# Performance work log

Hardware: AMD Instinct MI355X
Metric: run time of the kernel (lower is better)

The kernel has to match this reference:

```python
import jax, jax.numpy as jnp
import numpy as np

RX = 2  # matches init rx
RY = 2  # matches init ry


def _bilinear_gather(img, coords):
    """Bilinear sample with zero padding (mirrors grid_sample align_corners=True, padding_mode='zeros').
    img: [C,H,W]; coords: [P,2] pixel-space (x,y). Returns [C,P]."""
    C, H, W = img.shape
    x, y = coords[:, 0], coords[:, 1]
    x0, y0 = jnp.floor(x), jnp.floor(y)
    wx, wy = x - x0, y - y0

    def tap(xi, yi, w):
        valid = (xi >= 0) & (xi <= W - 1) & (yi >= 0) & (yi <= H - 1)
        xc = jnp.clip(xi, 0, W - 1).astype(jnp.int32)
        yc = jnp.clip(yi, 0, H - 1).astype(jnp.int32)
        v = img[:, yc, xc]  # [C,P] gather
        return v * (w * valid.astype(w.dtype))[None, :]

    return (tap(x0, y0, (1 - wx) * (1 - wy)) + tap(x0 + 1, y0, wx * (1 - wy))
            + tap(x0, y0 + 1, (1 - wx) * wy) + tap(x0 + 1, y0 + 1, wx * wy))


def _local_cost_volume(flow, f1, f2, rx, ry):
    """build_sample_cv: windowed bilinear gather of f2 around (grid + flow), dot with f1.
    Returns cv [N,H,W,2ry+1,2rx+1] with window ordered (dy,dx)."""
    N, C, H, W = f1.shape
    dt = f1.dtype
    gy, gx = jnp.meshgrid(jnp.arange(H, dtype=dt), jnp.arange(W, dtype=dt), indexing='ij')
    base = jnp.stack([gx, gy], 0)[None]            # [1,2,H,W] (x,y) like coords_grid
    cen = (base + flow).transpose(0, 2, 3, 1)       # [N,H,W,2]
    dx = jnp.linspace(-rx, rx, 2 * rx + 1).astype(dt)
    dy = jnp.linspace(-ry, ry, 2 * ry + 1).astype(dt)
    mgy, mgx = jnp.meshgrid(dy, dx, indexing='ij')  # [dH,dW]
    off = jnp.stack([mgx, mgy], -1)                 # [dH,dW,2] (x,y)
    dH, dW = 2 * ry + 1, 2 * rx + 1
    coords = cen[:, None, None] + off[None, :, :, None, None, :]  # [N,dH,dW,H,W,2]
    coords = coords.reshape(N, dH * dW * H * W, 2)
    samp = jax.vmap(_bilinear_gather)(f2, coords)   # [N,C,dH*dW*H*W]
    samp = samp.reshape(N, C, dH, dW, H, W)
    # cv[n,h,w,i,j] = sum_c f1[n,c,h,w] * f2_sampled[n,c,i,j,h,w]
    cv = jnp.einsum('nchw,ncijhw->nhwij', f1, samp)
    return cv


def setup_inputs() -> dict:
    key = jax.random.key(0)
    k1, k2, k3 = jax.random.split(key, 3)
    N, C, H, W = 2, 256, 55, 128
    return {
        'flow': jax.random.normal(k1, (N, 2, H, W), dtype=jnp.float32),
        'f1': jax.random.normal(k2, (N, C, H, W), dtype=jnp.float32),
        'f2': jax.random.normal(k3, (N, C, H, W), dtype=jnp.float32),
    }


def reference(flow, f1, f2):
    cv = _local_cost_volume(flow, f1, f2, RX, RY)   # [N,H,W,dH,dW]
    N, H, W, dH, dW = cv.shape
    flat = cv.reshape(N, H, W, dH * dW)
    # WTA over the last two (window) dims, as in get_argmax_NHW_xy_last_th
    wta_val = jnp.max(flat, axis=-1)
    idx = jnp.argmax(flat, axis=-1)
    wta_xy = jnp.stack([idx % dW, idx // dW], axis=0)  # [2,N,H,W] (x,y)
    return cv, wta_val, wta_xy
```

## Files before the change

### kernel.cpp

```cpp
#include <hip/hip_runtime.h>

#define N_   2
#define C_   256
#define H_   55
#define W_   128
#define HW_  (H_ * W_)
#define NPIX (N_ * HW_)
#define NBLK (NPIX / 4)
#define BPX  (NBLK / 8)

#define OFF_CV  0
#define OFF_VAL (NPIX * 25)
#define OFF_XY  (OFF_VAL + NPIX)

__global__ __launch_bounds__(256) void transpose_f2(const float* __restrict__ f2,
                                                    float* __restrict__ f2t) {
    __shared__ float tile[64][65];
    const int n = blockIdx.z;
    const float* __restrict__ src = f2 + (size_t)n * C_ * HW_;
    float* __restrict__ dst = f2t + (size_t)n * HW_ * C_;

    const int p0 = blockIdx.x * 64;
    const int c0 = blockIdx.y * 64;
    const int q = threadIdx.x & 15;
    const int r = threadIdx.x >> 4;

    #pragma unroll
    for (int rr = r; rr < 64; rr += 16) {
        const float4 v = *(const float4*)(src + (size_t)(c0 + rr) * HW_ + p0 + q * 4);
        tile[rr][q * 4 + 0] = v.x;
        tile[rr][q * 4 + 1] = v.y;
        tile[rr][q * 4 + 2] = v.z;
        tile[rr][q * 4 + 3] = v.w;
    }
    __syncthreads();

    #pragma unroll
    for (int j = 0; j < 4; ++j) {
        const int pr = r + 16 * j;
        float4 v;
        v.x = tile[q * 4 + 0][pr];
        v.y = tile[q * 4 + 1][pr];
        v.z = tile[q * 4 + 2][pr];
        v.w = tile[q * 4 + 3][pr];
        *(float4*)(dst + (size_t)(p0 + pr) * C_ + c0 + q * 4) = v;
    }
}

__device__ __forceinline__ float dot4(const float4 a, const float4 b) {
    return a.x * b.x + a.y * b.y + a.z * b.z + a.w * b.w;
}

__global__ __launch_bounds__(256) void costvol_kernel(const float* __restrict__ flow,
                                                      const float* __restrict__ f1,
                                                      const float* __restrict__ f2t,
                                                      float* __restrict__ out) {
    __shared__ float f1sh[4][C_];
    __shared__ float Dsh[4][36];

    const int b    = blockIdx.x;
    const int xcd  = b & 7;
    const int k    = b >> 3;
    const int pix0 = (xcd * BPX + k) * 4;
    const int n     = pix0 / HW_;
    const int prem0 = pix0 - n * HW_;

    {
        const int t = threadIdx.x;
        const float4 v = *(const float4*)(f1 + ((size_t)n * C_ + t) * HW_ + prem0);
        f1sh[0][t] = v.x;
        f1sh[1][t] = v.y;
        f1sh[2][t] = v.z;
        f1sh[3][t] = v.w;
    }

    const int wv   = threadIdx.x >> 6;
    const int lane = threadIdx.x & 63;
    const int sgrp = lane >> 4;
    const int cgrp = lane & 15;
    const int pix  = pix0 + wv;
    const int rem  = prem0 + wv;
    const int h    = rem >> 7;
    const int w    = rem & (W_ - 1);

    const float fx = flow[((size_t)(n * 2 + 0) * H_ + h) * W_ + w];
    const float fy = flow[((size_t)(n * 2 + 1) * H_ + h) * W_ + w];
    const float cx = (float)w + fx;
    const float cy = (float)h + fy;
    const float x0f = floorf(cx), y0f = floorf(cy);
    const float wx = cx - x0f,   wy = cy - y0f;
    const int ix0 = (int)x0f,    iy0 = (int)y0f;

    __syncthreads();

    const float4* __restrict__ arow = (const float4*)&f1sh[wv][cgrp * 16];
    const float4 a0 = arow[0], a1 = arow[1], a2 = arow[2], a3 = arow[3];

    const float4* __restrict__ f2base =
        (const float4*)(f2t + (size_t)n * HW_ * C_);

    #pragma unroll
    for (int p = 0; p < 9; ++p) {
        const int s  = p * 4 + sgrp;
        const int ly = s / 6, lx = s - ly * 6;
        const int sy = iy0 - 2 + ly;
        const int sx = ix0 - 2 + lx;
        float part = 0.f;
        if (sy >= 0 && sy < H_ && sx >= 0 && sx < W_) {
            const float4* __restrict__ bptr =
                f2base + (size_t)(sy * W_ + sx) * (C_ / 4) + cgrp * 4;
            part = dot4(a0, bptr[0]) + dot4(a1, bptr[1])
                 + dot4(a2, bptr[2]) + dot4(a3, bptr[3]);
        }
        part += __shfl_xor(part, 1, 64);
        part += __shfl_xor(part, 2, 64);
        part += __shfl_xor(part, 4, 64);
        part += __shfl_xor(part, 8, 64);
        if (cgrp == 0) Dsh[wv][s] = part;
    }
    __syncthreads();

    float cv = 0.f;
    if (lane < 25) {
        const int i = lane / 5, j = lane - i * 5;
        const float D00 = Dsh[wv][i * 6 + j];
        const float D01 = Dsh[wv][i * 6 + j + 1];
        const float D10 = Dsh[wv][i * 6 + j + 6];
        const float D11 = Dsh[wv][i * 6 + j + 7];
        cv = (1.f - wx) * (1.f - wy) * D00 + wx * (1.f - wy) * D01
           + (1.f - wx) * wy * D10 + wx * wy * D11;
        out[OFF_CV + (size_t)pix * 25 + lane] = cv;
    }

    float v  = (lane < 25) ? cv : -3.4e38f;
    int  idx = (lane < 25) ? lane : 25;
    #pragma unroll
    for (int off = 16; off >= 1; off >>= 1) {
        const float v2 = __shfl_down(v, off, 32);
        const int   i2 = __shfl_down(idx, off, 32);
        if (v2 > v || (v2 == v && i2 < idx)) { v = v2; idx = i2; }
    }
    if (lane == 0) {
        out[OFF_VAL + pix] = v;
        out[OFF_XY + pix]        = (float)(idx % 5);
        out[OFF_XY + NPIX + pix] = (float)(idx / 5);
    }
}

extern "C" void kernel_launch(void* const* d_in, const int* in_sizes, int n_in,
                              void* d_out, int out_size, void* d_ws, size_t ws_size,
                              hipStream_t stream) {
    const float* flow = (const float*)d_in[0];
    const float* f1   = (const float*)d_in[1];
    const float* f2   = (const float*)d_in[2];
    float* out = (float*)d_out;

    float* f2t = (float*)d_ws;

    transpose_f2<<<dim3(HW_ / 64, C_ / 64, N_), 256, 0, stream>>>(f2, f2t);
    costvol_kernel<<<dim3(NBLK), 256, 0, stream>>>(flow, f1, f2t, out);
}
```

Measured before the change: 111.7 us.

## Process 16 pixels per block with 4 pixels per wave and wave-level barriers

```diff
diff --git a/kernel.cpp b/kernel.cpp
--- a/kernel.cpp
+++ b/kernel.cpp
@@ -6,8 +6,11 @@
 #define W_   128
 #define HW_  (H_ * W_)
 #define NPIX (N_ * HW_)
-#define NBLK (NPIX / 4)
+#define PB   16
+#define PW   4
+#define NBLK (NPIX / PB)
 #define BPX  (NBLK / 8)
+#define F1LD 260
 
 #define OFF_CV  0
 #define OFF_VAL (NPIX * 25)
@@ -55,95 +58,107 @@
                                                       const float* __restrict__ f1,
                                                       const float* __restrict__ f2t,
                                                       float* __restrict__ out) {
-    __shared__ float f1sh[4][C_];
+    __shared__ float f1sh[PB][F1LD];
     __shared__ float Dsh[4][36];
 
     const int b    = blockIdx.x;
     const int xcd  = b & 7;
-    const int k    = b >> 3;
-    const int pix0 = (xcd * BPX + k) * 4;
+    const int kk   = b >> 3;
+    const int pix0 = (xcd * BPX + kk) * PB;
     const int n     = pix0 / HW_;
     const int prem0 = pix0 - n * HW_;
+    const int h     = prem0 >> 7;
+    const int w0    = prem0 & (W_ - 1);
 
     {
-        const int t = threadIdx.x;
-        const float4 v = *(const float4*)(f1 + ((size_t)n * C_ + t) * HW_ + prem0);
-        f1sh[0][t] = v.x;
-        f1sh[1][t] = v.y;
-        f1sh[2][t] = v.z;
-        f1sh[3][t] = v.w;
+        const int px4   = threadIdx.x & 3;
+        const int cbase = threadIdx.x >> 2;
+        #pragma unroll
+        for (int it = 0; it < 4; ++it) {
+            const int c = cbase + it * 64;
+            const float4 v = *(const float4*)(f1 + ((size_t)n * C_ + c) * HW_ + prem0 + px4 * 4);
+            f1sh[px4 * 4 + 0][c] = v.x;
+            f1sh[px4 * 4 + 1][c] = v.y;
+            f1sh[px4 * 4 + 2][c] = v.z;
+            f1sh[px4 * 4 + 3][c] = v.w;
+        }
     }
+    __syncthreads();
 
     const int wv   = threadIdx.x >> 6;
     const int lane = threadIdx.x & 63;
     const int sgrp = lane >> 4;
     const int cgrp = lane & 15;
-    const int pix  = pix0 + wv;
-    const int rem  = prem0 + wv;
-    const int h    = rem >> 7;
-    const int w    = rem & (W_ - 1);
 
-    const float fx = flow[((size_t)(n * 2 + 0) * H_ + h) * W_ + w];
-    const float fy = flow[((size_t)(n * 2 + 1) * H_ + h) * W_ + w];
-    const float cx = (float)w + fx;
-    const float cy = (float)h + fy;
-    const float x0f = floorf(cx), y0f = floorf(cy);
-    const float wx = cx - x0f,   wy = cy - y0f;
-    const int ix0 = (int)x0f,    iy0 = (int)y0f;
+    const float4* __restrict__ f2base = (const float4*)(f2t + (size_t)n * HW_ * C_);
+    const float* __restrict__ flown   = flow + (size_t)n * 2 * HW_;
 
-    __syncthreads();
+    for (int pp = 0; pp < PW; ++pp) {
+        const int pl  = wv * PW + pp;
+        const int pix = pix0 + pl;
+        const int w   = w0 + pl;
 
-    const float4* __restrict__ arow = (const float4*)&f1sh[wv][cgrp * 16];
-    const float4 a0 = arow[0], a1 = arow[1], a2 = arow[2], a3 = arow[3];
+        const float fx = flown[h * W_ + w];
+        const float fy = flown[HW_ + h * W_ + w];
+        const float cx = (float)w + fx;
+        const float cy = (float)h + fy;
+        const float x0f = floorf(cx), y0f = floorf(cy);
+        const float wx = cx - x0f, wy = cy - y0f;
+        const int ix0 = (int)x0f, iy0 = (int)y0f;
 
-    const float4* __restrict__ f2base =
-        (const float4*)(f2t + (size_t)n * HW_ * C_);
+        const float* fr = &f1sh[pl][cgrp * 4];
+        const float4 a0 = *(const float4*)(fr);
+        const float4 a1 = *(const float4*)(fr + 64);
+        const float4 a2 = *(const float4*)(fr + 128);
+        const float4 a3 = *(const float4*)(fr + 192);
 
-    #pragma unroll
-    for (int p = 0; p < 9; ++p) {
-        const int s  = p * 4 + sgrp;
-        const int ly = s / 6, lx = s - ly * 6;
-        const int sy = iy0 - 2 + ly;
-        const int sx = ix0 - 2 + lx;
-        float part = 0.f;
-        if (sy >= 0 && sy < H_ && sx >= 0 && sx < W_) {
-            const float4* __restrict__ bptr =
-                f2base + (size_t)(sy * W_ + sx) * (C_ / 4) + cgrp * 4;
-            part = dot4(a0, bptr[0]) + dot4(a1, bptr[1])
-                 + dot4(a2, bptr[2]) + dot4(a3, bptr[3]);
+        #pragma unroll
+        for (int p = 0; p < 9; ++p) {
+            const int s  = p * 4 + sgrp;
+            const int ly = s / 6, lx = s - ly * 6;
+            const int sy = iy0 - 2 + ly;
+            const int sx = ix0 - 2 + lx;
+            float part = 0.f;
+            if (sy >= 0 && sy < H_ && sx >= 0 && sx < W_) {
+                const float4* __restrict__ bp =
+                    f2base + (size_t)(sy * W_ + sx) * (C_ / 4) + cgrp;
+                part = dot4(a0, bp[0]) + dot4(a1, bp[16])
+                     + dot4(a2, bp[32]) + dot4(a3, bp[48]);
+            }
+            part += __shfl_xor(part, 1, 64);
+            part += __shfl_xor(part, 2, 64);
+            part += __shfl_xor(part, 4, 64);
+            part += __shfl_xor(part, 8, 64);
+            if (cgrp == 0) Dsh[wv][s] = part;
         }
-        part += __shfl_xor(part, 1, 64);
-        part += __shfl_xor(part, 2, 64);
-        part += __shfl_xor(part, 4, 64);
-        part += __shfl_xor(part, 8, 64);
-        if (cgrp == 0) Dsh[wv][s] = part;
-    }
-    __syncthreads();
+        __builtin_amdgcn_wave_barrier();
 
-    float cv = 0.f;
-    if (lane < 25) {
-        const int i = lane / 5, j = lane - i * 5;
-        const float D00 = Dsh[wv][i * 6 + j];
-        const float D01 = Dsh[wv][i * 6 + j + 1];
-        const float D10 = Dsh[wv][i * 6 + j + 6];
-        const float D11 = Dsh[wv][i * 6 + j + 7];
-        cv = (1.f - wx) * (1.f - wy) * D00 + wx * (1.f - wy) * D01
-           + (1.f - wx) * wy * D10 + wx * wy * D11;
-        out[OFF_CV + (size_t)pix * 25 + lane] = cv;
-    }
+        float cv = 0.f;
+        if (lane < 25) {
+            const int i = lane / 5, j = lane - i * 5;
+            const float D00 = Dsh[wv][i * 6 + j];
+            const float D01 = Dsh[wv][i * 6 + j + 1];
+            const float D10 = Dsh[wv][i * 6 + j + 6];
+            const float D11 = Dsh[wv][i * 6 + j + 7];
+            cv = (1.f - wx) * (1.f - wy) * D00 + wx * (1.f - wy) * D01
+               + (1.f - wx) * wy * D10 + wx * wy * D11;
+            out[OFF_CV + (size_t)pix * 25 + lane] = cv;
+        }
 
-    float v  = (lane < 25) ? cv : -3.4e38f;
-    int  idx = (lane < 25) ? lane : 25;
-    #pragma unroll
-    for (int off = 16; off >= 1; off >>= 1) {
-        const float v2 = __shfl_down(v, off, 32);
-        const int   i2 = __shfl_down(idx, off, 32);
-        if (v2 > v || (v2 == v && i2 < idx)) { v = v2; idx = i2; }
-    }
-    if (lane == 0) {
-        out[OFF_VAL + pix] = v;
-        out[OFF_XY + pix]        = (float)(idx % 5);
-        out[OFF_XY + NPIX + pix] = (float)(idx / 5);
+        float v  = (lane < 25) ? cv : -3.4e38f;
+        int  idx = (lane < 25) ? lane : 25;
+        #pragma unroll
+        for (int off = 16; off >= 1; off >>= 1) {
+            const float v2 = __shfl_down(v, off, 32);
+            const int   i2 = __shfl_down(idx, off, 32);
+            if (v2 > v || (v2 == v && i2 < idx)) { v = v2; idx = i2; }
+        }
+        if (lane == 0) {
+            out[OFF_VAL + pix] = v;
+            out[OFF_XY + pix]        = (float)(idx % 5);
+            out[OFF_XY + NPIX + pix] = (float)(idx / 5);
+        }
+        __builtin_amdgcn_wave_barrier();
     }
 }
 
```

Result: faster. 103.5 us (-7.3%).
